# Optimization experiments

Hardware: AMD Instinct MI355X
Metric: run time of the kernel (lower is better)

Reference implementation:

```python
import jax, jax.numpy as jnp
import numpy as np
from jax import lax

DN = ('NCHW', 'OIHW', 'NCHW')
EPS = 1e-9
MASK_THR = 1e-3


def box_filter(x, size):
    # Separable box (ones) filter with SAME padding; x: [1,1,H,W]
    pad = size // 2
    kv = jnp.ones((1, 1, size, 1), x.dtype)
    kh = jnp.ones((1, 1, 1, size), x.dtype)
    y = lax.conv_general_dilated(x, kv, (1, 1), [(pad, pad), (0, 0)], dimension_numbers=DN)
    return lax.conv_general_dilated(y, kh, (1, 1), [(0, 0), (pad, pad)], dimension_numbers=DN)


def setup_inputs() -> dict:
    key = jax.random.key(0)
    k1, k2, k3, k4 = jax.random.split(key, 4)
    H = W = 2048
    I = jax.random.uniform(k1, (1, 1, H, W), jnp.float32)            # image in [0,1]
    u = jax.random.uniform(k2, (1, 4, H, W), jnp.float32)            # class memberships
    b = 1.0 + 0.1 * jax.random.normal(k3, (1, 1, H, W), jnp.float32)  # bias field ~1
    e = jax.random.normal(k4, (1, 1, H, W), jnp.float32) * 0.1       # residual
    return {"I": I, "u": u, "b": b, "e": e, "p": 2, "size": 21}


def reference(I, u, b, e, p, size):
    C = u.shape[1]
    e_d = lax.stop_gradient(e)
    b_d = lax.stop_gradient(b)
    up = u ** p                      # [1,C,H,W]
    b2 = b_d * b_d
    mask = (I > MASK_THR).astype(I.dtype)
    norm = box_filter(mask, size)    # partialFilter: local valid-pixel count

    def filt(x):                     # convParFilt: mask-normalized local mean
        return box_filter(x, size) / (norm + EPS)

    b_K = filt(b)
    b2_K = filt(b2)

    # classCenter (vectorized over classes 1..C-1)
    A = (I - e_d) * b_K                                   # [1,1,H,W]
    num = jnp.sum(A * up[:, 1:], axis=(0, 2, 3))          # [C-1]
    den = jnp.sum(b2_K * up[:, 1:], axis=(0, 2, 3))       # [C-1]
    c0 = jnp.sum(I * up[:, :1]) / (jnp.sum(up[:, :1]) + EPS)
    v = jnp.concatenate([c0[None], num / (den + EPS)])    # [C]

    # bias-field update: convolution is linear, so sum over classes first
    vb = v[None, :, None, None]
    bd = filt((I - e_d) * jnp.sum(vb * up, axis=1, keepdims=True))
    db = filt(jnp.sum(vb * vb * up, axis=1, keepdims=True))
    bd = bd * mask + (1.0 - mask)
    db = db * mask + (1.0 - mask)
    b_new = bd / (db + EPS)
    diff = b - b_new
    return jnp.mean(diff * diff)
```

## Files before the change

kernel.cpp:

```cpp
#include <hip/hip_runtime.h>

constexpr int Hh = 2048;
constexpr int Ww = 2048;
constexpr int NN = Hh * Ww;
constexpr int W4 = Ww / 4;
constexpr int NN4 = NN / 4;
constexpr int RAD = 10;
constexpr float EPSf = 1e-9f;
constexpr float MASK_THRf = 0.001f;
constexpr int BH = 16;
constexpr int NB = Hh / BH;
constexpr int TOTW = NB * Ww;
constexpr int SEGW = 58;
constexpr int NSEG = 9;
constexpr int HBLOCKS = Hh * NSEG / 4;

__device__ inline float rcpf(float x) { return __builtin_amdgcn_rcpf(x); }

__device__ inline float waveReduce(float v) {
    #pragma unroll
    for (int o = 32; o > 0; o >>= 1) v += __shfl_down(v, o, 64);
    return v;
}

__device__ inline float4 f4zero() { float4 z; z.x = z.y = z.z = z.w = 0.f; return z; }
__device__ inline float4 f4add(float4 a, float4 b) {
    float4 r; r.x = a.x + b.x; r.y = a.y + b.y; r.z = a.z + b.z; r.w = a.w + b.w; return r;
}
__device__ inline float4 f4sub(float4 a, float4 b) {
    float4 r; r.x = a.x - b.x; r.y = a.y - b.y; r.z = a.z - b.z; r.w = a.w - b.w; return r;
}
__device__ inline void add4(float4& a, const float4 b) { a.x += b.x; a.y += b.y; a.z += b.z; a.w += b.w; }

__device__ inline float4 hbox(float4 v, int lane) {
    float S = v.x + v.y + v.z + v.w;
    float Sm2 = __shfl(S, lane - 2, 64);
    float Sm1 = __shfl(S, lane - 1, 64);
    float Sp1 = __shfl(S, lane + 1, 64);
    float Sp2 = __shfl(S, lane + 2, 64);
    float T5 = Sm2 + Sm1 + S + Sp1 + Sp2;
    float wm3 = __shfl(v.w, lane - 3, 64);
    float zm3 = __shfl(v.z, lane - 3, 64);
    float xm2 = __shfl(v.x, lane - 2, 64);
    float wp2 = __shfl(v.w, lane + 2, 64);
    float xp3 = __shfl(v.x, lane + 3, 64);
    float yp3 = __shfl(v.y, lane + 3, 64);
    float4 r;
    r.y = T5 + wm3;
    r.z = T5 + xp3;
    r.x = r.y + zm3 - wp2;
    r.w = r.z + yp3 - xm2;
    return r;
}

__global__ __launch_bounds__(256) void k1p(
        const float* __restrict__ I, const float* __restrict__ B,
        float* __restrict__ vpm, float* __restrict__ vpb, float* __restrict__ vpb2,
        float* __restrict__ tm, float* __restrict__ tb, float* __restrict__ tb2) {
    int x4 = blockIdx.x * 256 + threadIdx.x;
    int y0 = blockIdx.y * BH;
    const float4* I4 = (const float4*)I;
    const float4* B4 = (const float4*)B;
    float4 am = f4zero(), ab = f4zero(), ab2 = f4zero();
    #pragma unroll
    for (int r = 0; r < BH; ++r) {
        int idx = (y0 + r) * W4 + x4;
        float4 iv = I4[idx], bv = B4[idx];
        am.x += (iv.x > MASK_THRf) ? 1.f : 0.f;
        am.y += (iv.y > MASK_THRf) ? 1.f : 0.f;
        am.z += (iv.z > MASK_THRf) ? 1.f : 0.f;
        am.w += (iv.w > MASK_THRf) ? 1.f : 0.f;
        ab.x += bv.x; ab.y += bv.y; ab.z += bv.z; ab.w += bv.w;
        ab2.x += bv.x * bv.x; ab2.y += bv.y * bv.y;
        ab2.z += bv.z * bv.z; ab2.w += bv.w * bv.w;
        ((float4*)vpm)[idx] = am;
        ((float4*)vpb)[idx] = ab;
        ((float4*)vpb2)[idx] = ab2;
    }
    int t = blockIdx.y * W4 + x4;
    ((float4*)tm)[t] = am; ((float4*)tb)[t] = ab; ((float4*)tb2)[t] = ab2;
}

__global__ __launch_bounds__(256) void koff(
        const float* __restrict__ t0, const float* __restrict__ t1, const float* __restrict__ t2,
        float* __restrict__ o0, float* __restrict__ o1, float* __restrict__ o2) {
    int col = blockIdx.x * 256 + threadIdx.x;
    const float4* t; float4* o;
    if (blockIdx.y == 0)      { t = (const float4*)t0; o = (float4*)o0; }
    else if (blockIdx.y == 1) { t = (const float4*)t1; o = (float4*)o1; }
    else                      { t = (const float4*)t2; o = (float4*)o2; }
    float4 acc = f4zero();
    #pragma unroll 8
    for (int b = 0; b < NB; ++b) {
        o[b * W4 + col] = acc;
        float4 v = t[b * W4 + col];
        add4(acc, v);
    }
}

__device__ inline void k2_pix(float bm, float bb, float bb2, float Iv, float ev,
                              float u0, float u1, float u2, float u3, float* a) {
    float rn = rcpf(bm + EPSf);
    float bK = bb * rn;
    float b2K = bb2 * rn;
    float p0 = u0 * u0, p1 = u1 * u1, p2 = u2 * u2, p3 = u3 * u3;
    a[0] += Iv * p0;
    a[1] += p0;
    float A = (Iv - ev) * bK;
    a[2] += A * p1; a[3] += A * p2; a[4] += A * p3;
    a[5] += b2K * p1; a[6] += b2K * p2; a[7] += b2K * p3;
}

__global__ __launch_bounds__(256) void k2s(
        const float* __restrict__ vpm, const float* __restrict__ vpb, const float* __restrict__ vpb2,
        const float* __restrict__ om, const float* __restrict__ ob, const float* __restrict__ ob2,
        const float* __restrict__ I, const float* __restrict__ E, const float* __restrict__ U,
        float* __restrict__ partA) {
    int lane = threadIdx.x & 63;
    int wid = blockIdx.x * 4 + (threadIdx.x >> 6);
    int row = wid / NSEG;
    int seg = wid - row * NSEG;
    int xc = seg * SEGW - 3 + lane;
    bool inb = (unsigned)xc < (unsigned)W4;
    int xl = inb ? xc : 0;

    int yup = row + RAD; if (yup > Hh - 1) yup = Hh - 1;
    int ydn = row - RAD - 1;
    bool hasDn = ydn >= 0;
    int upBase = yup * W4 + xl;
    int dnBase = (hasDn ? ydn * W4 : 0) + xl;
    int obUp = (yup / BH) * W4 + xl;
    int obDn = (hasDn ? (ydn / BH) * W4 : 0) + xl;

    const float4* Pm = (const float4*)vpm;
    const float4* Pb = (const float4*)vpb;
    const float4* Pq = (const float4*)vpb2;
    const float4* Om = (const float4*)om;
    const float4* Ob = (const float4*)ob;
    const float4* Oq = (const float4*)ob2;

    float4 vm = f4zero(), vb = f4zero(), vq = f4zero();
    if (inb) {
        vm = f4add(Pm[upBase], Om[obUp]);
        vb = f4add(Pb[upBase], Ob[obUp]);
        vq = f4add(Pq[upBase], Oq[obUp]);
        if (hasDn) {
            vm = f4sub(vm, f4add(Pm[dnBase], Om[obDn]));
            vb = f4sub(vb, f4add(Pb[dnBase], Ob[obDn]));
            vq = f4sub(vq, f4add(Pq[dnBase], Oq[obDn]));
        }
    }

    float4 bm = hbox(vm, lane);
    float4 bb = hbox(vb, lane);
    float4 bq = hbox(vq, lane);

    float a[8] = {0, 0, 0, 0, 0, 0, 0, 0};
    if (inb && lane >= 3 && lane <= 60) {
        const float4* I4 = (const float4*)I;
        const float4* E4 = (const float4*)E;
        const float4* U0 = (const float4*)U;
        const float4* U1 = U0 + NN4;
        const float4* U2 = U1 + NN4;
        const float4* U3 = U2 + NN4;
        int xo = row * W4 + xc;
        float4 Iv = I4[xo], Ev = E4[xo];
        float4 u0 = U0[xo], u1 = U1[xo], u2 = U2[xo], u3 = U3[xo];
        k2_pix(bm.x, bb.x, bq.x, Iv.x, Ev.x, u0.x, u1.x, u2.x, u3.x, a);
        k2_pix(bm.y, bb.y, bq.y, Iv.y, Ev.y, u0.y, u1.y, u2.y, u3.y, a);
        k2_pix(bm.z, bb.z, bq.z, Iv.z, Ev.z, u0.z, u1.z, u2.z, u3.z, a);
        k2_pix(bm.w, bb.w, bq.w, Iv.w, Ev.w, u0.w, u1.w, u2.w, u3.w, a);
    }

    __shared__ float sred[4][8];
    int wave = threadIdx.x >> 6;
    #pragma unroll
    for (int k = 0; k < 8; ++k) a[k] = waveReduce(a[k]);
    if (lane == 0) {
        #pragma unroll
        for (int k = 0; k < 8; ++k) sred[wave][k] = a[k];
    }
    __syncthreads();
    if (threadIdx.x < 8) {
        float s = sred[0][threadIdx.x] + sred[1][threadIdx.x] +
                  sred[2][threadIdx.x] + sred[3][threadIdx.x];
        partA[(blockIdx.x << 3) + threadIdx.x] = s;
    }
}

__global__ __launch_bounds__(1024) void k3_v(const float* __restrict__ partA, float* __restrict__ vV) {
    __shared__ float s[1024];
    int tid = threadIdx.x;
    float acc = 0.f;
    #pragma unroll
    for (int j = 0; j < (HBLOCKS * 8) / 1024; ++j) acc += partA[tid + j * 1024];
    s[tid] = acc;
    __syncthreads();
    #pragma unroll
    for (int st = 512; st >= 8; st >>= 1) {
        if (tid < st) s[tid] += s[tid + st];
        __syncthreads();
    }
    if (tid == 0) {
        vV[0] = s[0] / (s[1] + EPSf);
        vV[1] = s[2] / (s[5] + EPSf);
        vV[2] = s[3] / (s[6] + EPSf);
        vV[3] = s[4] / (s[7] + EPSf);
    }
}

__global__ __launch_bounds__(256) void k4p(
        const float* __restrict__ I, const float* __restrict__ E, const float* __restrict__ U,
        const float* __restrict__ vV,
        float* __restrict__ vpP, float* __restrict__ vpQ,
        float* __restrict__ tP, float* __restrict__ tQ) {
    int x4 = blockIdx.x * 256 + threadIdx.x;
    int y0 = blockIdx.y * BH;
    float v0 = vV[0], v1 = vV[1], v2 = vV[2], v3 = vV[3];
    float w0 = v0 * v0, w1 = v1 * v1, w2 = v2 * v2, w3 = v3 * v3;
    const float4* I4 = (const float4*)I;
    const float4* E4 = (const float4*)E;
    const float4* U0 = (const float4*)U;
    const float4* U1 = U0 + NN4;
    const float4* U2 = U1 + NN4;
    const float4* U3 = U2 + NN4;
    float4 aP = f4zero(), aQ = f4zero();
    #pragma unroll
    for (int r = 0; r < BH; ++r) {
        int idx = (y0 + r) * W4 + x4;
        float4 Iv = I4[idx], Ev = E4[idx];
        float4 a0 = U0[idx], a1 = U1[idx], a2 = U2[idx], a3 = U3[idx];
        float p0, p1, p2, p3;
        p0 = a0.x * a0.x; p1 = a1.x * a1.x; p2 = a2.x * a2.x; p3 = a3.x * a3.x;
        aP.x += (Iv.x - Ev.x) * (v0 * p0 + v1 * p1 + v2 * p2 + v3 * p3);
        aQ.x += w0 * p0 + w1 * p1 + w2 * p2 + w3 * p3;
        p0 = a0.y * a0.y; p1 = a1.y * a1.y; p2 = a2.y * a2.y; p3 = a3.y * a3.y;
        aP.y += (Iv.y - Ev.y) * (v0 * p0 + v1 * p1 + v2 * p2 + v3 * p3);
        aQ.y += w0 * p0 + w1 * p1 + w2 * p2 + w3 * p3;
        p0 = a0.z * a0.z; p1 = a1.z * a1.z; p2 = a2.z * a2.z; p3 = a3.z * a3.z;
        aP.z += (Iv.z - Ev.z) * (v0 * p0 + v1 * p1 + v2 * p2 + v3 * p3);
        aQ.z += w0 * p0 + w1 * p1 + w2 * p2 + w3 * p3;
        p0 = a0.w * a0.w; p1 = a1.w * a1.w; p2 = a2.w * a2.w; p3 = a3.w * a3.w;
        aP.w += (Iv.w - Ev.w) * (v0 * p0 + v1 * p1 + v2 * p2 + v3 * p3);
        aQ.w += w0 * p0 + w1 * p1 + w2 * p2 + w3 * p3;
        ((float4*)vpP)[idx] = aP;
        ((float4*)vpQ)[idx] = aQ;
    }
    int t = blockIdx.y * W4 + x4;
    ((float4*)tP)[t] = aP; ((float4*)tQ)[t] = aQ;
}

__global__ __launch_bounds__(256) void k5s(
        const float* __restrict__ vpP, const float* __restrict__ vpQ, const float* __restrict__ vpm,
        const float* __restrict__ oP, const float* __restrict__ oQ, const float* __restrict__ om,
        const float* __restrict__ I, const float* __restrict__ B,
        float* __restrict__ partL) {
    int lane = threadIdx.x & 63;
    int wid = blockIdx.x * 4 + (threadIdx.x >> 6);
    int row = wid / NSEG;
    int seg = wid - row * NSEG;
    int xc = seg * SEGW - 3 + lane;
    bool inb = (unsigned)xc < (unsigned)W4;
    int xl = inb ? xc : 0;

    int yup = row + RAD; if (yup > Hh - 1) yup = Hh - 1;
    int ydn = row - RAD - 1;
    bool hasDn = ydn >= 0;
    int upBase = yup * W4 + xl;
    int dnBase = (hasDn ? ydn * W4 : 0) + xl;
    int obUp = (yup / BH) * W4 + xl;
    int obDn = (hasDn ? (ydn / BH) * W4 : 0) + xl;

    const float4* Pp4 = (const float4*)vpP;
    const float4* Pq4 = (const float4*)vpQ;
    const float4* Pm4 = (const float4*)vpm;
    const float4* Op4 = (const float4*)oP;
    const float4* Oq4 = (const float4*)oQ;
    const float4* Om4 = (const float4*)om;

    float4 vP = f4zero(), vQ = f4zero(), vM = f4zero();
    if (inb) {
        vP = f4add(Pp4[upBase], Op4[obUp]);
        vQ = f4add(Pq4[upBase], Oq4[obUp]);
        vM = f4add(Pm4[upBase], Om4[obUp]);
        if (hasDn) {
            vP = f4sub(vP, f4add(Pp4[dnBase], Op4[obDn]));
            vQ = f4sub(vQ, f4add(Pq4[dnBase], Oq4[obDn]));
            vM = f4sub(vM, f4add(Pm4[dnBase], Om4[obDn]));
        }
    }

    float4 bP = hbox(vP, lane);
    float4 bQ = hbox(vQ, lane);
    float4 bM = hbox(vM, lane);

    float a = 0.f;
    if (inb && lane >= 3 && lane <= 60) {
        const float4* I4 = (const float4*)I;
        const float4* B4 = (const float4*)B;
        int xo = row * W4 + xc;
        float4 Iv = I4[xo], Bv = B4[xo];
        {
            float rn = rcpf(bM.x + EPSf);
            float bd = bP.x * rn, db = bQ.x * rn;
            float m = (Iv.x > MASK_THRf) ? 1.f : 0.f;
            bd = bd * m + (1.f - m); db = db * m + (1.f - m);
            float d = Bv.x - bd * rcpf(db + EPSf); a += d * d;
        }
        {
            float rn = rcpf(bM.y + EPSf);
            float bd = bP.y * rn, db = bQ.y * rn;
            float m = (Iv.y > MASK_THRf) ? 1.f : 0.f;
            bd = bd * m + (1.f - m); db = db * m + (1.f - m);
            float d = Bv.y - bd * rcpf(db + EPSf); a += d * d;
        }
        {
            float rn = rcpf(bM.z + EPSf);
            float bd = bP.z * rn, db = bQ.z * rn;
            float m = (Iv.z > MASK_THRf) ? 1.f : 0.f;
            bd = bd * m + (1.f - m); db = db * m + (1.f - m);
            float d = Bv.z - bd * rcpf(db + EPSf); a += d * d;
        }
        {
            float rn = rcpf(bM.w + EPSf);
            float bd = bP.w * rn, db = bQ.w * rn;
            float m = (Iv.w > MASK_THRf) ? 1.f : 0.f;
            bd = bd * m + (1.f - m); db = db * m + (1.f - m);
            float d = Bv.w - bd * rcpf(db + EPSf); a += d * d;
        }
    }

    a = waveReduce(a);
    __shared__ float sred[4];
    int wave = threadIdx.x >> 6;
    if (lane == 0) sred[wave] = a;
    __syncthreads();
    if (threadIdx.x == 0) {
        partL[blockIdx.x] = sred[0] + sred[1] + sred[2] + sred[3];
    }
}

__global__ __launch_bounds__(1024) void k6_out(const float* __restrict__ partL, float* __restrict__ out) {
    __shared__ float s[1024];
    int tid = threadIdx.x;
    float acc = 0.f;
    for (int c = tid; c < HBLOCKS; c += 1024) acc += partL[c];
    s[tid] = acc;
    __syncthreads();
    #pragma unroll
    for (int st = 512; st >= 1; st >>= 1) {
        if (tid < st) s[tid] += s[tid + st];
        __syncthreads();
    }
    if (tid == 0) out[0] = s[0] / (float)NN;
}

extern "C" void kernel_launch(void* const* d_in, const int* in_sizes, int n_in,
                              void* d_out, int out_size, void* d_ws, size_t ws_size,
                              hipStream_t stream) {
    const float* I = (const float*)d_in[0];
    const float* U = (const float*)d_in[1];
    const float* B = (const float*)d_in[2];
    const float* E = (const float*)d_in[3];

    float* vpm  = (float*)d_ws;
    float* vpb  = vpm + NN;
    float* vpb2 = vpb + NN;
    float* tm   = vpb2 + NN;
    float* tb   = tm + TOTW;
    float* tb2  = tb + TOTW;
    float* om   = tb2 + TOTW;
    float* ob   = om + TOTW;
    float* ob2  = ob + TOTW;
    float* vV   = ob2 + TOTW;

    float* partA = tm;
    float* partL = tb2;

    dim3 blk(256);
    dim3 gband(2, NB);

    k1p<<<gband, blk, 0, stream>>>(I, B, vpm, vpb, vpb2, tm, tb, tb2);
    koff<<<dim3(2, 3), blk, 0, stream>>>(tm, tb, tb2, om, ob, ob2);
    k2s<<<HBLOCKS, blk, 0, stream>>>(vpm, vpb, vpb2, om, ob, ob2, I, E, U, partA);
    k3_v<<<1, 1024, 0, stream>>>(partA, vV);
    k4p<<<gband, blk, 0, stream>>>(I, E, U, vV, vpb, vpb2, tm, tb);
    koff<<<dim3(2, 2), blk, 0, stream>>>(tm, tb, tb2, ob, ob2, om);
    k5s<<<HBLOCKS, blk, 0, stream>>>(vpb, vpb2, vpm, ob, ob2, om, I, B, partL);
    k6_out<<<1, 1024, 0, stream>>>(partL, (float*)d_out);
}
```

Measured before the change: 232.4 us.

## Make k2s/k5s persistent with double-buffered software-pipelined loads across row segments

The two horizontal-box reduction kernels now launch 512 blocks instead of one wave per item, and each wave loops over 9 work items. Loads for the next item are issued into a second register buffer while the current item is computed. Per-wave partials are written directly, removing the block-level shared-memory reduction and __syncthreads. The aim is to hide global-memory latency and cut launch/tail overhead, at the cost of much higher register pressure from two large load structs, which may lower occupancy.

```diff
diff --git a/kernel.cpp b/kernel.cpp
--- a/kernel.cpp
+++ b/kernel.cpp
@@ -13,7 +13,12 @@
 constexpr int TOTW = NB * Ww;
 constexpr int SEGW = 58;
 constexpr int NSEG = 9;
-constexpr int HBLOCKS = Hh * NSEG / 4;
+constexpr int TOTIT = Hh * NSEG;
+constexpr int PBLK = 512;
+constexpr int PWAVES = PBLK * 4;
+constexpr int ITPW = TOTIT / PWAVES;
+
+static_assert(ITPW * PWAVES == TOTIT, "exact item division required");
 
 __device__ inline float rcpf(float x) { return __builtin_amdgcn_rcpf(x); }
 
@@ -111,6 +116,63 @@
     a[5] += b2K * p1; a[6] += b2K * p2; a[7] += b2K * p3;
 }
 
+struct It2 {
+    float4 mU, bU, qU, mD, bD, qD;
+    float4 oMU, oBU, oQU, oMD, oBD, oQD;
+    float4 iv, ev, u0, u1, u2, u3;
+};
+
+__device__ inline void load2(int it, int lane,
+        const float4* Pm, const float4* Pb, const float4* Pq,
+        const float4* Om, const float4* Ob, const float4* Oq,
+        const float4* I4, const float4* E4,
+        const float4* U0, const float4* U1, const float4* U2, const float4* U3,
+        It2& t) {
+    int row = it / NSEG;
+    int seg = it - row * NSEG;
+    int xc = seg * SEGW - 3 + lane;
+    bool inb = (unsigned)xc < (unsigned)W4;
+    int xl = inb ? xc : 0;
+    int yup = row + RAD; if (yup > Hh - 1) yup = Hh - 1;
+    int ydn = row - RAD - 1;
+    int ydc = (ydn >= 0) ? ydn : 0;
+    int upB = yup * W4 + xl, dnB = ydc * W4 + xl;
+    int oU = (yup / BH) * W4 + xl, oD = (ydc / BH) * W4 + xl;
+    int xo = row * W4 + xl;
+    t.mU = Pm[upB]; t.bU = Pb[upB]; t.qU = Pq[upB];
+    t.mD = Pm[dnB]; t.bD = Pb[dnB]; t.qD = Pq[dnB];
+    t.oMU = Om[oU]; t.oBU = Ob[oU]; t.oQU = Oq[oU];
+    t.oMD = Om[oD]; t.oBD = Ob[oD]; t.oQD = Oq[oD];
+    t.iv = I4[xo];  t.ev = E4[xo];
+    t.u0 = U0[xo];  t.u1 = U1[xo];  t.u2 = U2[xo]; t.u3 = U3[xo];
+}
+
+__device__ inline void comp2(int it, int lane, const It2& t, float* a) {
+    int row = it / NSEG;
+    int seg = it - row * NSEG;
+    int xc = seg * SEGW - 3 + lane;
+    bool inb = (unsigned)xc < (unsigned)W4;
+    bool hasDn = row >= RAD + 1;
+    float4 vm = f4add(t.mU, t.oMU);
+    float4 vb = f4add(t.bU, t.oBU);
+    float4 vq = f4add(t.qU, t.oQU);
+    if (hasDn) {
+        vm = f4sub(vm, f4add(t.mD, t.oMD));
+        vb = f4sub(vb, f4add(t.bD, t.oBD));
+        vq = f4sub(vq, f4add(t.qD, t.oQD));
+    }
+    if (!inb) { vm = f4zero(); vb = f4zero(); vq = f4zero(); }
+    float4 bm = hbox(vm, lane);
+    float4 bb = hbox(vb, lane);
+    float4 bq = hbox(vq, lane);
+    if (inb && lane >= 3 && lane <= 60) {
+        k2_pix(bm.x, bb.x, bq.x, t.iv.x, t.ev.x, t.u0.x, t.u1.x, t.u2.x, t.u3.x, a);
+        k2_pix(bm.y, bb.y, bq.y, t.iv.y, t.ev.y, t.u0.y, t.u1.y, t.u2.y, t.u3.y, a);
+        k2_pix(bm.z, bb.z, bq.z, t.iv.z, t.ev.z, t.u0.z, t.u1.z, t.u2.z, t.u3.z, a);
+        k2_pix(bm.w, bb.w, bq.w, t.iv.w, t.ev.w, t.u0.w, t.u1.w, t.u2.w, t.u3.w, a);
+    }
+}
+
 __global__ __launch_bounds__(256) void k2s(
         const float* __restrict__ vpm, const float* __restrict__ vpb, const float* __restrict__ vpb2,
         const float* __restrict__ om, const float* __restrict__ ob, const float* __restrict__ ob2,
@@ -118,19 +180,6 @@
         float* __restrict__ partA) {
     int lane = threadIdx.x & 63;
     int wid = blockIdx.x * 4 + (threadIdx.x >> 6);
-    int row = wid / NSEG;
-    int seg = wid - row * NSEG;
-    int xc = seg * SEGW - 3 + lane;
-    bool inb = (unsigned)xc < (unsigned)W4;
-    int xl = inb ? xc : 0;
-
-    int yup = row + RAD; if (yup > Hh - 1) yup = Hh - 1;
-    int ydn = row - RAD - 1;
-    bool hasDn = ydn >= 0;
-    int upBase = yup * W4 + xl;
-    int dnBase = (hasDn ? ydn * W4 : 0) + xl;
-    int obUp = (yup / BH) * W4 + xl;
-    int obDn = (hasDn ? (ydn / BH) * W4 : 0) + xl;
 
     const float4* Pm = (const float4*)vpm;
     const float4* Pb = (const float4*)vpb;
@@ -138,53 +187,33 @@
     const float4* Om = (const float4*)om;
     const float4* Ob = (const float4*)ob;
     const float4* Oq = (const float4*)ob2;
-
-    float4 vm = f4zero(), vb = f4zero(), vq = f4zero();
-    if (inb) {
-        vm = f4add(Pm[upBase], Om[obUp]);
-        vb = f4add(Pb[upBase], Ob[obUp]);
-        vq = f4add(Pq[upBase], Oq[obUp]);
-        if (hasDn) {
-            vm = f4sub(vm, f4add(Pm[dnBase], Om[obDn]));
-            vb = f4sub(vb, f4add(Pb[dnBase], Ob[obDn]));
-            vq = f4sub(vq, f4add(Pq[dnBase], Oq[obDn]));
-        }
-    }
-
-    float4 bm = hbox(vm, lane);
-    float4 bb = hbox(vb, lane);
-    float4 bq = hbox(vq, lane);
+    const float4* I4 = (const float4*)I;
+    const float4* E4 = (const float4*)E;
+    const float4* U0 = (const float4*)U;
+    const float4* U1 = U0 + NN4;
+    const float4* U2 = U1 + NN4;
+    const float4* U3 = U2 + NN4;
 
     float a[8] = {0, 0, 0, 0, 0, 0, 0, 0};
-    if (inb && lane >= 3 && lane <= 60) {
-        const float4* I4 = (const float4*)I;
-        const float4* E4 = (const float4*)E;
-        const float4* U0 = (const float4*)U;
-        const float4* U1 = U0 + NN4;
-        const float4* U2 = U1 + NN4;
-        const float4* U3 = U2 + NN4;
-        int xo = row * W4 + xc;
-        float4 Iv = I4[xo], Ev = E4[xo];
-        float4 u0 = U0[xo], u1 = U1[xo], u2 = U2[xo], u3 = U3[xo];
-        k2_pix(bm.x, bb.x, bq.x, Iv.x, Ev.x, u0.x, u1.x, u2.x, u3.x, a);
-        k2_pix(bm.y, bb.y, bq.y, Iv.y, Ev.y, u0.y, u1.y, u2.y, u3.y, a);
-        k2_pix(bm.z, bb.z, bq.z, Iv.z, Ev.z, u0.z, u1.z, u2.z, u3.z, a);
-        k2_pix(bm.w, bb.w, bq.w, Iv.w, Ev.w, u0.w, u1.w, u2.w, u3.w, a);
-    }
-
-    __shared__ float sred[4][8];
-    int wave = threadIdx.x >> 6;
+    It2 A, B;
+    load2(wid, lane, Pm, Pb, Pq, Om, Ob, Oq, I4, E4, U0, U1, U2, U3, A);
+    #pragma unroll
+    for (int k = 0; k < 4; ++k) {
+        load2(wid + (2 * k + 1) * PWAVES, lane, Pm, Pb, Pq, Om, Ob, Oq, I4, E4, U0, U1, U2, U3, B);
+        comp2(wid + (2 * k) * PWAVES, lane, A, a);
+        load2(wid + (2 * k + 2) * PWAVES, lane, Pm, Pb, Pq, Om, Ob, Oq, I4, E4, U0, U1, U2, U3, A);
+        comp2(wid + (2 * k + 1) * PWAVES, lane, B, a);
+    }
+    comp2(wid + 8 * PWAVES, lane, A, a);
+
     #pragma unroll
     for (int k = 0; k < 8; ++k) a[k] = waveReduce(a[k]);
     if (lane == 0) {
-        #pragma unroll
-        for (int k = 0; k < 8; ++k) sred[wave][k] = a[k];
-    }
-    __syncthreads();
-    if (threadIdx.x < 8) {
-        float s = sred[0][threadIdx.x] + sred[1][threadIdx.x] +
-                  sred[2][threadIdx.x] + sred[3][threadIdx.x];
-        partA[(blockIdx.x << 3) + threadIdx.x] = s;
+        float4 r0, r1;
+        r0.x = a[0]; r0.y = a[1]; r0.z = a[2]; r0.w = a[3];
+        r1.x = a[4]; r1.y = a[5]; r1.z = a[6]; r1.w = a[7];
+        ((float4*)partA)[wid * 2]     = r0;
+        ((float4*)partA)[wid * 2 + 1] = r1;
     }
 }
 
@@ -193,7 +222,7 @@
     int tid = threadIdx.x;
     float acc = 0.f;
     #pragma unroll
-    for (int j = 0; j < (HBLOCKS * 8) / 1024; ++j) acc += partA[tid + j * 1024];
+    for (int j = 0; j < (PWAVES * 8) / 1024; ++j) acc += partA[tid + j * 1024];
     s[tid] = acc;
     __syncthreads();
     #pragma unroll
@@ -250,6 +279,84 @@
     ((float4*)tP)[t] = aP; ((float4*)tQ)[t] = aQ;
 }
 
+struct It5 {
+    float4 pU, qU, mU, pD, qD, mD;
+    float4 oPU, oQU, oMU, oPD, oQD, oMD;
+    float4 iv, bv;
+};
+
+__device__ inline void load5(int it, int lane,
+        const float4* Pp, const float4* Pq, const float4* Pm,
+        const float4* Op, const float4* Oq, const float4* Om,
+        const float4* I4, const float4* B4, It5& t) {
+    int row = it / NSEG;
+    int seg = it - row * NSEG;
+    int xc = seg * SEGW - 3 + lane;
+    bool inb = (unsigned)xc < (unsigned)W4;
+    int xl = inb ? xc : 0;
+    int yup = row + RAD; if (yup > Hh - 1) yup = Hh - 1;
+    int ydn = row - RAD - 1;
+    int ydc = (ydn >= 0) ? ydn : 0;
+    int upB = yup * W4 + xl, dnB = ydc * W4 + xl;
+    int oU = (yup / BH) * W4 + xl, oD = (ydc / BH) * W4 + xl;
+    int xo = row * W4 + xl;
+    t.pU = Pp[upB]; t.qU = Pq[upB]; t.mU = Pm[upB];
+    t.pD = Pp[dnB]; t.qD = Pq[dnB]; t.mD = Pm[dnB];
+    t.oPU = Op[oU]; t.oQU = Oq[oU]; t.oMU = Om[oU];
+    t.oPD = Op[oD]; t.oQD = Oq[oD]; t.oMD = Om[oD];
+    t.iv = I4[xo];  t.bv = B4[xo];
+}
+
+__device__ inline void comp5(int it, int lane, const It5& t, float& a) {
+    int row = it / NSEG;
+    int seg = it - row * NSEG;
+    int xc = seg * SEGW - 3 + lane;
+    bool inb = (unsigned)xc < (unsigned)W4;
+    bool hasDn = row >= RAD + 1;
+    float4 vP = f4add(t.pU, t.oPU);
+    float4 vQ = f4add(t.qU, t.oQU);
+    float4 vM = f4add(t.mU, t.oMU);
+    if (hasDn) {
+        vP = f4sub(vP, f4add(t.pD, t.oPD));
+        vQ = f4sub(vQ, f4add(t.qD, t.oQD));
+        vM = f4sub(vM, f4add(t.mD, t.oMD));
+    }
+    if (!inb) { vP = f4zero(); vQ = f4zero(); vM = f4zero(); }
+    float4 bP = hbox(vP, lane);
+    float4 bQ = hbox(vQ, lane);
+    float4 bM = hbox(vM, lane);
+    if (inb && lane >= 3 && lane <= 60) {
+        {
+            float rn = rcpf(bM.x + EPSf);
+            float bd = bP.x * rn, db = bQ.x * rn;
+            float m = (t.iv.x > MASK_THRf) ? 1.f : 0.f;
+            bd = bd * m + (1.f - m); db = db * m + (1.f - m);
+            float d = t.bv.x - bd * rcpf(db + EPSf); a += d * d;
+        }
+        {
+            float rn = rcpf(bM.y + EPSf);
+            float bd = bP.y * rn, db = bQ.y * rn;
+            float m = (t.iv.y > MASK_THRf) ? 1.f : 0.f;
+            bd = bd * m + (1.f - m); db = db * m + (1.f - m);
+            float d = t.bv.y - bd * rcpf(db + EPSf); a += d * d;
+        }
+        {
+            float rn = rcpf(bM.z + EPSf);
+            float bd = bP.z * rn, db = bQ.z * rn;
+            float m = (t.iv.z > MASK_THRf) ? 1.f : 0.f;
+            bd = bd * m + (1.f - m); db = db * m + (1.f - m);
+            float d = t.bv.z - bd * rcpf(db + EPSf); a += d * d;
+        }
+        {
+            float rn = rcpf(bM.w + EPSf);
+            float bd = bP.w * rn, db = bQ.w * rn;
+            float m = (t.iv.w > MASK_THRf) ? 1.f : 0.f;
+            bd = bd * m + (1.f - m); db = db * m + (1.f - m);
+            float d = t.bv.w - bd * rcpf(db + EPSf); a += d * d;
+        }
+    }
+}
+
 __global__ __launch_bounds__(256) void k5s(
         const float* __restrict__ vpP, const float* __restrict__ vpQ, const float* __restrict__ vpm,
         const float* __restrict__ oP, const float* __restrict__ oQ, const float* __restrict__ om,
@@ -257,94 +364,37 @@
         float* __restrict__ partL) {
     int lane = threadIdx.x & 63;
     int wid = blockIdx.x * 4 + (threadIdx.x >> 6);
-    int row = wid / NSEG;
-    int seg = wid - row * NSEG;
-    int xc = seg * SEGW - 3 + lane;
-    bool inb = (unsigned)xc < (unsigned)W4;
-    int xl = inb ? xc : 0;
-
-    int yup = row + RAD; if (yup > Hh - 1) yup = Hh - 1;
-    int ydn = row - RAD - 1;
-    bool hasDn = ydn >= 0;
-    int upBase = yup * W4 + xl;
-    int dnBase = (hasDn ? ydn * W4 : 0) + xl;
-    int obUp = (yup / BH) * W4 + xl;
-    int obDn = (hasDn ? (ydn / BH) * W4 : 0) + xl;
-
-    const float4* Pp4 = (const float4*)vpP;
-    const float4* Pq4 = (const float4*)vpQ;
-    const float4* Pm4 = (const float4*)vpm;
-    const float4* Op4 = (const float4*)oP;
-    const float4* Oq4 = (const float4*)oQ;
-    const float4* Om4 = (const float4*)om;
-
-    float4 vP = f4zero(), vQ = f4zero(), vM = f4zero();
-    if (inb) {
-        vP = f4add(Pp4[upBase], Op4[obUp]);
-        vQ = f4add(Pq4[upBase], Oq4[obUp]);
-        vM = f4add(Pm4[upBase], Om4[obUp]);
-        if (hasDn) {
-            vP = f4sub(vP, f4add(Pp4[dnBase], Op4[obDn]));
-            vQ = f4sub(vQ, f4add(Pq4[dnBase], Oq4[obDn]));
-            vM = f4sub(vM, f4add(Pm4[dnBase], Om4[obDn]));
-        }
-    }
-
-    float4 bP = hbox(vP, lane);
-    float4 bQ = hbox(vQ, lane);
-    float4 bM = hbox(vM, lane);
+
+    const float4* Pp = (const float4*)vpP;
+    const float4* Pq = (const float4*)vpQ;
+    const float4* Pm = (const float4*)vpm;
+    const float4* Op = (const float4*)oP;
+    const float4* Oq = (const float4*)oQ;
+    const float4* Om = (const float4*)om;
+    const float4* I4 = (const float4*)I;
+    const float4* B4 = (const float4*)B;
 
     float a = 0.f;
-    if (inb && lane >= 3 && lane <= 60) {
-        const float4* I4 = (const float4*)I;
-        const float4* B4 = (const float4*)B;
-        int xo = row * W4 + xc;
-        float4 Iv = I4[xo], Bv = B4[xo];
-        {
-            float rn = rcpf(bM.x + EPSf);
-            float bd = bP.x * rn, db = bQ.x * rn;
-            float m = (Iv.x > MASK_THRf) ? 1.f : 0.f;
-            bd = bd * m + (1.f - m); db = db * m + (1.f - m);
-            float d = Bv.x - bd * rcpf(db + EPSf); a += d * d;
-        }
-        {
-            float rn = rcpf(bM.y + EPSf);
-            float bd = bP.y * rn, db = bQ.y * rn;
-            float m = (Iv.y > MASK_THRf) ? 1.f : 0.f;
-            bd = bd * m + (1.f - m); db = db * m + (1.f - m);
-            float d = Bv.y - bd * rcpf(db + EPSf); a += d * d;
-        }
-        {
-            float rn = rcpf(bM.z + EPSf);
-            float bd = bP.z * rn, db = bQ.z * rn;
-            float m = (Iv.z > MASK_THRf) ? 1.f : 0.f;
-            bd = bd * m + (1.f - m); db = db * m + (1.f - m);
-            float d = Bv.z - bd * rcpf(db + EPSf); a += d * d;
-        }
-        {
-            float rn = rcpf(bM.w + EPSf);
-            float bd = bP.w * rn, db = bQ.w * rn;
-            float m = (Iv.w > MASK_THRf) ? 1.f : 0.f;
-            bd = bd * m + (1.f - m); db = db * m + (1.f - m);
-            float d = Bv.w - bd * rcpf(db + EPSf); a += d * d;
-        }
-    }
+    It5 A, B2;
+    load5(wid, lane, Pp, Pq, Pm, Op, Oq, Om, I4, B4, A);
+    #pragma unroll
+    for (int k = 0; k < 4; ++k) {
+        load5(wid + (2 * k + 1) * PWAVES, lane, Pp, Pq, Pm, Op, Oq, Om, I4, B4, B2);
+        comp5(wid + (2 * k) * PWAVES, lane, A, a);
+        load5(wid + (2 * k + 2) * PWAVES, lane, Pp, Pq, Pm, Op, Oq, Om, I4, B4, A);
+        comp5(wid + (2 * k + 1) * PWAVES, lane, B2, a);
+    }
+    comp5(wid + 8 * PWAVES, lane, A, a);
 
     a = waveReduce(a);
-    __shared__ float sred[4];
-    int wave = threadIdx.x >> 6;
-    if (lane == 0) sred[wave] = a;
-    __syncthreads();
-    if (threadIdx.x == 0) {
-        partL[blockIdx.x] = sred[0] + sred[1] + sred[2] + sred[3];
-    }
+    if (lane == 0) partL[wid] = a;
 }
 
 __global__ __launch_bounds__(1024) void k6_out(const float* __restrict__ partL, float* __restrict__ out) {
     __shared__ float s[1024];
     int tid = threadIdx.x;
     float acc = 0.f;
-    for (int c = tid; c < HBLOCKS; c += 1024) acc += partL[c];
+    for (int c = tid; c < PWAVES; c += 1024) acc += partL[c];
     s[tid] = acc;
     __syncthreads();
     #pragma unroll
@@ -382,10 +432,10 @@
 
     k1p<<<gband, blk, 0, stream>>>(I, B, vpm, vpb, vpb2, tm, tb, tb2);
     koff<<<dim3(2, 3), blk, 0, stream>>>(tm, tb, tb2, om, ob, ob2);
-    k2s<<<HBLOCKS, blk, 0, stream>>>(vpm, vpb, vpb2, om, ob, ob2, I, E, U, partA);
+    k2s<<<PBLK, blk, 0, stream>>>(vpm, vpb, vpb2, om, ob, ob2, I, E, U, partA);
     k3_v<<<1, 1024, 0, stream>>>(partA, vV);
     k4p<<<gband, blk, 0, stream>>>(I, E, U, vV, vpb, vpb2, tm, tb);
     koff<<<dim3(2, 2), blk, 0, stream>>>(tm, tb, tb2, ob, ob2, om);
-    k5s<<<HBLOCKS, blk, 0, stream>>>(vpb, vpb2, vpm, ob, ob2, om, I, B, partL);
+    k5s<<<PBLK, blk, 0, stream>>>(vpb, vpb2, vpm, ob, ob2, om, I, B, partL);
     k6_out<<<1, 1024, 0, stream>>>(partL, (float*)d_out);
 }
```

Result: no change. 235.3 us (+1.2%).
